# Performance work log

Hardware: AMD Instinct MI355X
Metric: run time of the kernel (lower is better)

The kernel has to match this reference:

```python
import jax, jax.numpy as jnp
import numpy as np

N, E, F_IN, C, H, L, G, OUT = 10000, 120000, 64, 128, 4, 5, 500, 1801
HL = (L * C) // 2  # JK bidirectional LSTM hidden per direction = 320


def setup_inputs():
    key = jax.random.key(0)
    ks = jax.random.split(key, 20)
    s = 0.05
    p = {}
    p["x"] = jax.random.normal(ks[0], (N, F_IN), jnp.float32)
    p["edge_index"] = jax.random.randint(ks[1], (2, E), 0, N)
    p["batch"] = jnp.sort(jax.random.randint(ks[2], (N,), 0, G))
    p["emb_W"] = jax.random.normal(ks[3], (F_IN, C)) * s
    p["emb_b"] = jnp.zeros((C,))
    p["Wl"] = jax.random.normal(ks[4], (L, C, H * C)) * s
    p["bl"] = jnp.zeros((L, H * C))
    p["Wr"] = jax.random.normal(ks[5], (L, C, H * C)) * s
    p["br"] = jnp.zeros((L, H * C))
    p["att_a"] = jax.random.normal(ks[6], (L, H, C)) * s
    p["conv_b"] = jnp.zeros((L, C))
    p["ln_w"] = jnp.ones((L, C))
    p["ln_b"] = jnp.zeros((L, C))
    p["Wih_f"] = jax.random.normal(ks[7], (4 * HL, C)) * s
    p["Whh_f"] = jax.random.normal(ks[8], (4 * HL, HL)) * s
    p["bih_f"] = jnp.zeros((4 * HL,))
    p["bhh_f"] = jnp.zeros((4 * HL,))
    p["Wih_b"] = jax.random.normal(ks[9], (4 * HL, C)) * s
    p["Whh_b"] = jax.random.normal(ks[10], (4 * HL, HL)) * s
    p["bih_b"] = jnp.zeros((4 * HL,))
    p["bhh_b"] = jnp.zeros((4 * HL,))
    p["jk_w"] = jax.random.normal(ks[11], (2 * HL,)) * s
    p["jk_b"] = jnp.zeros(())
    p["m1_w"] = jax.random.normal(ks[12], (C, C)) * s
    p["m1_b"] = jnp.zeros((C,))
    p["m2_w"] = jax.random.normal(ks[13], (C, OUT)) * s
    p["m2_b"] = jnp.zeros((OUT,))
    p["res_w"] = jax.random.normal(ks[14], (C, OUT)) * s
    p["res_b"] = jnp.zeros((OUT,))
    return p


def _layernorm(x, w, b):
    mu = x.mean(-1, keepdims=True)
    var = ((x - mu) ** 2).mean(-1, keepdims=True)
    return (x - mu) * jax.lax.rsqrt(var + 1e-5) * w + b


def _gatv2(x, src, dst, Wl, bl, Wr, br, a, bias):
    # GATv2Conv, concat=False: mean over heads; eval mode (no dropout)
    xl = (x @ Wl + bl).reshape(N, H, C)   # source projection
    xr = (x @ Wr + br).reshape(N, H, C)   # target projection
    xj = xl[src]                          # [E,H,C] messages from source
    e = jax.nn.leaky_relu(xj + xr[dst], 0.2)
    score = jnp.einsum('ehc,hc->eh', e, a)              # [E,H]
    m = jax.ops.segment_max(score, dst, num_segments=N)  # per-target max
    m = jnp.where(jnp.isfinite(m), m, 0.0)
    ex = jnp.exp(score - m[dst])
    denom = jax.ops.segment_sum(ex, dst, num_segments=N)
    alpha = ex / (denom[dst] + 1e-16)                   # PyG segment softmax
    out = jax.ops.segment_sum(xj * alpha[:, :, None], dst, num_segments=N)
    return out.mean(axis=1) + bias


def _lstm(seq, Wih, Whh, bih, bhh):
    # seq: [L, N, C]; torch gate order i,f,g,o
    def step(carry, xt):
        h, c = carry
        g = xt @ Wih.T + bih + h @ Whh.T + bhh
        i, f, gg, o = jnp.split(g, 4, axis=-1)
        c = jax.nn.sigmoid(f) * c + jax.nn.sigmoid(i) * jnp.tanh(gg)
        h = jax.nn.sigmoid(o) * jnp.tanh(c)
        return (h, c), h
    h0 = jnp.zeros((seq.shape[1], HL), seq.dtype)
    _, hs = jax.lax.scan(step, (h0, h0), seq)
    return hs


def reference(x, edge_index, batch, emb_W, emb_b, Wl, bl, Wr, br, att_a, conv_b, ln_w, ln_b, Wih_f, Whh_f, bih_f, bhh_f, Wih_b, Whh_b, bih_b, bhh_b, jk_w, jk_b, m1_w, m1_b, m2_w, m2_b, res_w, res_b):
    src, dst = edge_index[0], edge_index[1]
    h = x @ emb_W + emb_b
    xs = []
    for l in range(L):
        h = _gatv2(h, src, dst, Wl[l], bl[l], Wr[l], br[l], att_a[l], conv_b[l])
        h = _layernorm(h, ln_w[l], ln_b[l])
        xs.append(h)
    seq = jnp.stack(xs, axis=0)                           # [L,N,C]
    hf = _lstm(seq, Wih_f, Whh_f, bih_f, bhh_f)
    hb = _lstm(seq[::-1], Wih_b, Whh_b, bih_b, bhh_b)[::-1]
    feat = jnp.concatenate([hf, hb], axis=-1)             # [L,N,2*HL]
    scores = feat @ jk_w + jk_b                           # [L,N]
    alpha = jax.nn.softmax(scores, axis=0)
    node = (seq * alpha[:, :, None]).sum(axis=0)          # [N,C]
    cnt = jax.ops.segment_sum(jnp.ones((N,), node.dtype), batch, num_segments=G)
    pooled = jax.ops.segment_sum(node, batch, num_segments=G) / jnp.maximum(cnt, 1.0)[:, None]
    hdn = jax.nn.relu(pooled @ m1_w + m1_b)               # MLPBlock (eval: no dropout)
    return hdn @ m2_w + m2_b + pooled @ res_w + res_b
```

## Files before the change

kernel.cpp:

```cpp
#include <hip/hip_runtime.h>
#include <hip/hip_bf16.h>
#include <math.h>

constexpr int cN   = 10000;
constexpr int cE   = 120000;
constexpr int cFin = 64;
constexpr int cC   = 128;
constexpr int cH   = 4;
constexpr int cL   = 5;
constexpr int cG   = 500;
constexpr int cOUT = 1801;
constexpr int cHL  = 320;
constexpr int c4HL = 4 * cHL;

typedef short bf16x8 __attribute__((ext_vector_type(8)));
typedef float f32x4 __attribute__((ext_vector_type(4)));

__device__ inline unsigned short f2b(float x) {
    union { __hip_bfloat16 h; unsigned short u; } cv;
    cv.h = __float2bfloat16(x);
    return cv.u;
}
__device__ inline float b2f(unsigned short u) {
    union { unsigned int i; float f; } cv;
    cv.i = ((unsigned int)u) << 16;
    return cv.f;
}
__device__ inline float fsig(float x)  { return 1.f / (1.f + __expf(-x)); }
__device__ inline float ftanh(float x) { return 1.f - 2.f / (__expf(2.f * x) + 1.f); }

#define GLD16(g, l) __builtin_amdgcn_global_load_lds( \
    (const __attribute__((address_space(1))) unsigned int*)(g), \
    (__attribute__((address_space(3))) unsigned int*)(l), 16, 0, 0)

__global__ void fill_f32_kernel(float* __restrict__ p, long n, float v) {
    long i = (long)blockIdx.x * blockDim.x + threadIdx.x;
    if (i < n) p[i] = v;
}
__global__ void fill_i32_kernel(int* __restrict__ p, long n, int v) {
    long i = (long)blockIdx.x * blockDim.x + threadIdx.x;
    if (i < n) p[i] = v;
}
__global__ void copy_i32_kernel(const int* __restrict__ a, int* __restrict__ b, long n) {
    long i = (long)blockIdx.x * blockDim.x + threadIdx.x;
    if (i < n) b[i] = a[i];
}
__global__ void conv_bf16_kernel(const float* __restrict__ a, unsigned short* __restrict__ b, long n) {
    long i = (long)blockIdx.x * blockDim.x + threadIdx.x;
    if (i < n) b[i] = f2b(a[i]);
}
__global__ void wproj_prep_kernel(const float* __restrict__ Wl, const float* __restrict__ Wr,
                                  unsigned short* __restrict__ WT) {
    long i = (long)blockIdx.x * blockDim.x + threadIdx.x;
    if (i >= (long)cL * 1024 * 128) return;
    int k = i & 127;
    int n = (int)((i >> 7) & 1023);
    int l = (int)(i >> 17);
    const float* W = (n < 512) ? Wl : Wr;
    int nn = n & 511;
    WT[i] = f2b(W[(size_t)l * 65536 + (size_t)k * 512 + nn]);
}
__global__ void bias_prep_kernel(const float* __restrict__ bl, const float* __restrict__ br,
                                 float* __restrict__ bb) {
    int i = blockIdx.x * blockDim.x + threadIdx.x;
    if (i >= cL * 1024) return;
    int n = i & 1023, l = i >> 10;
    bb[i] = (n < 512) ? bl[l * 512 + n] : br[l * 512 + (n - 512)];
}
__global__ void embw_prep_kernel(const float* __restrict__ W, unsigned short* __restrict__ WT) {
    int i = blockIdx.x * blockDim.x + threadIdx.x;
    if (i >= cC * cFin) return;
    int k = i & 63, n = i >> 6;
    WT[i] = f2b(W[(size_t)k * cC + n]);
}
__global__ void lstm_prep_kernel(const float* __restrict__ Wih, const float* __restrict__ Whh,
                                 const float* __restrict__ bih, const float* __restrict__ bhh,
                                 unsigned short* __restrict__ WihP, unsigned short* __restrict__ WhhP,
                                 float* __restrict__ biasP) {
    long i = (long)blockIdx.x * blockDim.x + threadIdx.x;
    if (i >= (long)c4HL * 449) return;
    int p = (int)(i / 449), c = (int)(i % 449);
    int u = (p >> 6) * 16 + (p & 15);
    int g = (p >> 4) & 3;
    int r = g * cHL + u;
    if (c < cC)       WihP[(size_t)p * cC + c] = f2b(Wih[(size_t)r * cC + c]);
    else if (c < 448) WhhP[(size_t)p * cHL + (c - cC)] = f2b(Whh[(size_t)r * cHL + (c - cC)]);
    else              biasP[p] = bih[r] + bhh[r];
}

__global__ void hist_kernel(const int* __restrict__ dst, int* __restrict__ count) {
    int i = blockIdx.x * blockDim.x + threadIdx.x;
    if (i < cE) atomicAdd(&count[dst[i]], 1);
}
__global__ void scan_kernel(const int* __restrict__ count, int* __restrict__ offs) {
    __shared__ int part[256];
    const int tid = threadIdx.x;
    const int CH = (cN + 255) / 256;
    int base = tid * CH;
    int s = 0;
    for (int i = 0; i < CH; i++) {
        int idx = base + i;
        if (idx < cN) s += count[idx];
    }
    part[tid] = s;
    __syncthreads();
    for (int d = 1; d < 256; d <<= 1) {
        int v = 0;
        if (tid >= d) v = part[tid - d];
        __syncthreads();
        if (tid >= d) part[tid] += v;
        __syncthreads();
    }
    int prefix = (tid == 0) ? 0 : part[tid - 1];
    for (int i = 0; i < CH; i++) {
        int idx = base + i;
        if (idx < cN) { offs[idx] = prefix; prefix += count[idx]; }
    }
    if (tid == 255) offs[cN] = prefix;
}
__global__ void scatter_kernel(const int* __restrict__ src, const int* __restrict__ dst,
                               int* __restrict__ cursor, int* __restrict__ src_csr) {
    int i = blockIdx.x * blockDim.x + threadIdx.x;
    if (i < cE) {
        int pos = atomicAdd(&cursor[dst[i]], 1);
        src_csr[pos] = src[i];
    }
}

template<int HASBIAS, int OUTB, int SWZ>
__global__ __launch_bounds__(256)
void gemm_mfma_kernel(const unsigned short* __restrict__ A1, const unsigned short* __restrict__ B1, int k1,
                      const unsigned short* __restrict__ A2, const unsigned short* __restrict__ B2, int k2,
                      const float* __restrict__ bias, void* __restrict__ Cout, int M, int N, int nbn) {
    int bm, bn;
    if (SWZ) {
        int bid = blockIdx.x;
        int xcd = bid & 7, j = bid >> 3;
        int g   = (j / nbn) * 8 + xcd;
        bm = g << 7;
        bn = (j % nbn) << 7;
        if (bm >= M) return;
    } else {
        bm = blockIdx.y << 7;
        bn = blockIdx.x << 7;
    }
    __shared__ unsigned short lds[2][2][128 * 32];
    const int tid  = threadIdx.x;
    const int lane = tid & 63;
    const int wave = tid >> 6;
    const int wr = (wave >> 1) << 6;
    const int wc = (wave & 1) << 6;
    const int ns1 = k1 >> 5, ns2 = k2 >> 5, ns = ns1 + ns2;

    const int lrow = lane >> 2;
    const int lke  = (lane & 3) << 3;

    auto stage = [&](int s, int buf) {
        const unsigned short *Ab, *Bb;
        int stride, koff;
        if (s < ns1) { Ab = A1; Bb = B1; stride = k1; koff = s << 5; }
        else         { Ab = A2; Bb = B2; stride = k2; koff = (s - ns1) << 5; }
#pragma unroll
        for (int r = 0; r < 2; r++) {
            int ch  = wave * 2 + r;
            int row = ch * 16 + lrow;
            int ga  = bm + row; if (ga >= M) ga = M - 1;
            GLD16(Ab + (size_t)ga * stride + koff + lke, &lds[buf][0][ch * 512]);
            GLD16(Bb + (size_t)(bn + row) * stride + koff + lke, &lds[buf][1][ch * 512]);
        }
    };

    f32x4 acc[4][4];
#pragma unroll
    for (int i = 0; i < 4; i++)
#pragma unroll
        for (int j = 0; j < 4; j++) acc[i][j] = (f32x4){0.f, 0.f, 0.f, 0.f};

    stage(0, 0);
    const int ko  = (lane >> 4) << 3;
    const int rla = lane & 15;
    for (int s = 0; s < ns; s++) {
        int buf = s & 1;
        __syncthreads();
        if (s + 1 < ns) stage(s + 1, buf ^ 1);
        bf16x8 af[4], bff[4];
#pragma unroll
        for (int f = 0; f < 4; f++) {
            af[f]  = *(const bf16x8*)&lds[buf][0][(wr + f * 16 + rla) * 32 + ko];
            bff[f] = *(const bf16x8*)&lds[buf][1][(wc + f * 16 + rla) * 32 + ko];
        }
#pragma unroll
        for (int i = 0; i < 4; i++)
#pragma unroll
            for (int j = 0; j < 4; j++)
                acc[i][j] = __builtin_amdgcn_mfma_f32_16x16x32_bf16(af[i], bff[j], acc[i][j], 0, 0, 0);
    }

#pragma unroll
    for (int i = 0; i < 4; i++) {
#pragma unroll
        for (int v = 0; v < 4; v++) {
            int m = bm + wr + i * 16 + ((lane >> 4) << 2) + v;
            if (m < M) {
#pragma unroll
                for (int j = 0; j < 4; j++) {
                    int n = bn + wc + j * 16 + rla;
                    float val = acc[i][j][v];
                    if (HASBIAS) val += bias[n];
                    if (OUTB) ((unsigned short*)Cout)[(size_t)m * N + n] = f2b(val);
                    else      ((float*)Cout)[(size_t)m * N + n] = val;
                }
            }
        }
    }
}

template<int FIRST>
__global__ __launch_bounds__(512)
void gemm_lstm_dual_kernel(const unsigned short* __restrict__ A1f, const unsigned short* __restrict__ A1b,
                           const unsigned short* __restrict__ Bihf, const unsigned short* __restrict__ Bihb,
                           const unsigned short* __restrict__ A2f, const unsigned short* __restrict__ A2b,
                           const unsigned short* __restrict__ Bhhf, const unsigned short* __restrict__ Bhhb,
                           const float* __restrict__ biasPf, const float* __restrict__ biasPb,
                           float* __restrict__ cff, float* __restrict__ cbb,
                           unsigned short* __restrict__ hOutf, unsigned short* __restrict__ hOutb,
                           const float* __restrict__ jkw,
                           float* __restrict__ scoref, float* __restrict__ scoreb) {
    constexpr int M = cN, k1 = cC, k2 = FIRST ? 0 : cHL;
    const int bid = blockIdx.x;
    const int xcd = bid & 7, jj = bid >> 3;
    const int g     = (jj / 10) * 8 + xcd;
    const int inner = jj % 10;
    const int bm = g << 7;
    if (bm >= M) return;
    const int bn = (inner % 5) << 8;
    const int z  = inner / 5;

    const unsigned short* A1 = z ? A1b : A1f;
    const unsigned short* B1 = z ? Bihb : Bihf;
    const unsigned short* A2 = z ? A2b : A2f;
    const unsigned short* B2 = z ? Bhhb : Bhhf;
    const float* biasP = z ? biasPb : biasPf;
    float* cbuf = z ? cbb : cff;
    unsigned short* hOut = z ? hOutb : hOutf;
    const float* jkwz = jkw + (z ? cHL : 0);
    float* score_t = z ? scoreb : scoref;

    __shared__ unsigned short ldsA[2][128 * 32];
    __shared__ unsigned short ldsB[2][256 * 32];
    const int tid  = threadIdx.x;
    const int lane = tid & 63;
    const int wave = tid >> 6;
    const int wr = (wave >> 2) << 6;
    const int wc = (wave & 3) << 6;
    const int ns1 = k1 >> 5, ns2 = k2 >> 5, ns = ns1 + ns2;

    const int lrow = lane >> 2;
    const int lke  = (lane & 3) << 3;

    auto stage = [&](int s, int buf) {
        const unsigned short *Ab, *Bb;
        int stride, koff;
        if (s < ns1) { Ab = A1; Bb = B1; stride = k1; koff = s << 5; }
        else         { Ab = A2; Bb = B2; stride = k2; koff = (s - ns1) << 5; }
        {
            int row = wave * 16 + lrow;
            int ga  = bm + row; if (ga >= M) ga = M - 1;
            GLD16(Ab + (size_t)ga * stride + koff + lke, &ldsA[buf][wave * 512]);
        }
#pragma unroll
        for (int r = 0; r < 2; r++) {
            int ch  = wave * 2 + r;
            int row = ch * 16 + lrow;
            GLD16(Bb + (size_t)(bn + row) * stride + koff + lke, &ldsB[buf][ch * 512]);
        }
    };

    f32x4 acc[4][4];
#pragma unroll
    for (int i = 0; i < 4; i++)
#pragma unroll
        for (int j = 0; j < 4; j++) acc[i][j] = (f32x4){0.f, 0.f, 0.f, 0.f};

    stage(0, 0);
    const int ko  = (lane >> 4) << 3;
    const int rla = lane & 15;
    for (int s = 0; s < ns; s++) {
        int buf = s & 1;
        __syncthreads();
        if (s + 1 < ns) stage(s + 1, buf ^ 1);
        bf16x8 af[4], bff[4];
#pragma unroll
        for (int f = 0; f < 4; f++) {
            af[f]  = *(const bf16x8*)&ldsA[buf][(wr + f * 16 + rla) * 32 + ko];
            bff[f] = *(const bf16x8*)&ldsB[buf][(wc + f * 16 + rla) * 32 + ko];
        }
#pragma unroll
        for (int i = 0; i < 4; i++)
#pragma unroll
            for (int j = 0; j < 4; j++)
                acc[i][j] = __builtin_amdgcn_mfma_f32_16x16x32_bf16(af[i], bff[j], acc[i][j], 0, 0, 0);
    }

    float bias4[4];
#pragma unroll
    for (int j = 0; j < 4; j++) bias4[j] = biasP[bn + wc + j * 16 + rla];
    const int u = ((bn + wc) >> 6) * 16 + rla;
    const float jw = jkwz[u];

#pragma unroll
    for (int i = 0; i < 4; i++) {
#pragma unroll
        for (int v = 0; v < 4; v++) {
            int m = bm + wr + i * 16 + ((lane >> 4) << 2) + v;
            bool ok = (m < M);
            float gi = acc[i][0][v] + bias4[0];
            float gf = acc[i][1][v] + bias4[1];
            float gg = acc[i][2][v] + bias4[2];
            float go = acc[i][3][v] + bias4[3];
            float si = fsig(gi);
            float sf = fsig(gf);
            float so = fsig(go);
            float tg = ftanh(gg);
            size_t idx = (size_t)m * cHL + u;
            float cold = (FIRST || !ok) ? 0.f : cbuf[idx];
            float cc = sf * cold + si * tg;
            float hh = so * ftanh(cc);
            if (ok) { cbuf[idx] = cc; hOut[idx] = f2b(hh); }
            float part = ok ? hh * jw : 0.f;
#pragma unroll
            for (int o = 1; o < 16; o <<= 1) part += __shfl_xor(part, o);
            if (rla == 0 && ok) atomicAdd(&score_t[m], part);
        }
    }
}

__global__ __launch_bounds__(256)
void gat_fused_kernel(const unsigned short* __restrict__ xlr, const int* __restrict__ src_csr,
                      const int* __restrict__ offs, const float* __restrict__ att,
                      const float* __restrict__ conv_b, const float* __restrict__ lnw,
                      const float* __restrict__ lnb, float* __restrict__ seq_l,
                      unsigned short* __restrict__ seqb_l) {
    const int wv   = (blockIdx.x * blockDim.x + threadIdx.x) >> 6;
    const int lane = threadIdx.x & 63;
    if (wv >= cN) return;
    const int h   = lane >> 4;
    const int cb  = (lane & 15) << 3;

    bf16x8 xrv = *(const bf16x8*)&xlr[(size_t)wv * 1024 + 512 + lane * 8];
    float xr[8], av[8];
#pragma unroll
    for (int k = 0; k < 8; k++) {
        xr[k] = b2f((unsigned short)xrv[k]);
        av[k] = att[h * 128 + cb + k];
    }

    float m = -INFINITY, l = 0.f;
    float acc[8];
#pragma unroll
    for (int k = 0; k < 8; k++) acc[k] = 0.f;

    const int beg = offs[wv], end = offs[wv + 1];
    int j = beg;
    for (; j + 1 < end; j += 2) {
        int s0 = src_csr[j], s1 = src_csr[j + 1];
        bf16x8 xv0 = *(const bf16x8*)&xlr[(size_t)s0 * 1024 + lane * 8];
        bf16x8 xv1 = *(const bf16x8*)&xlr[(size_t)s1 * 1024 + lane * 8];
        float x0[8], x1[8], sc0 = 0.f, sc1 = 0.f;
#pragma unroll
        for (int k = 0; k < 8; k++) {
            x0[k] = b2f((unsigned short)xv0[k]);
            float v0 = x0[k] + xr[k];
            v0 = v0 > 0.f ? v0 : 0.2f * v0;
            sc0 = fmaf(v0, av[k], sc0);
            x1[k] = b2f((unsigned short)xv1[k]);
            float v1 = x1[k] + xr[k];
            v1 = v1 > 0.f ? v1 : 0.2f * v1;
            sc1 = fmaf(v1, av[k], sc1);
        }
#pragma unroll
        for (int o = 1; o < 16; o <<= 1) {
            sc0 += __shfl_xor(sc0, o);
            sc1 += __shfl_xor(sc1, o);
        }
        float mn = fmaxf(m, fmaxf(sc0, sc1));
        float r  = __expf(m - mn);
        float p0 = __expf(sc0 - mn);
        float p1 = __expf(sc1 - mn);
        l = l * r + p0 + p1;
#pragma unroll
        for (int k = 0; k < 8; k++)
            acc[k] = fmaf(acc[k], r, fmaf(p0, x0[k], p1 * x1[k]));
        m = mn;
    }
    if (j < end) {
        int s0 = src_csr[j];
        bf16x8 xv = *(const bf16x8*)&xlr[(size_t)s0 * 1024 + lane * 8];
        float x[8], sc = 0.f;
#pragma unroll
        for (int k = 0; k < 8; k++) {
            x[k] = b2f((unsigned short)xv[k]);
            float v = x[k] + xr[k];
            v = v > 0.f ? v : 0.2f * v;
            sc = fmaf(v, av[k], sc);
        }
#pragma unroll
        for (int o = 1; o < 16; o <<= 1) sc += __shfl_xor(sc, o);
        float mn = fmaxf(m, sc);
        float r  = __expf(m - mn);
        float p  = __expf(sc - mn);
        l = l * r + p;
#pragma unroll
        for (int k = 0; k < 8; k++) acc[k] = fmaf(acc[k], r, p * x[k]);
        m = mn;
    }
    float inv = 1.f / (l + 1e-16f);

#pragma unroll
    for (int k = 0; k < 8; k++) {
        float v = acc[k] * inv;
        v += __shfl_xor(v, 16);
        v += __shfl_xor(v, 32);
        acc[k] = 0.25f * v + conv_b[cb + k];
    }
    float ssum = 0.f;
#pragma unroll
    for (int k = 0; k < 8; k++) ssum += acc[k];
#pragma unroll
    for (int o = 1; o < 16; o <<= 1) ssum += __shfl_xor(ssum, o);
    float mu = ssum * (1.f / 128.f);
    float vs = 0.f;
#pragma unroll
    for (int k = 0; k < 8; k++) { float d = acc[k] - mu; vs = fmaf(d, d, vs); }
#pragma unroll
    for (int o = 1; o < 16; o <<= 1) vs += __shfl_xor(vs, o);
    float rstd = 1.f / sqrtf(vs * (1.f / 128.f) + 1e-5f);

    float outv[8];
#pragma unroll
    for (int k = 0; k < 8; k++)
        outv[k] = (acc[k] - mu) * rstd * lnw[cb + k] + lnb[cb + k];

    if (h == 0) {
        size_t b = (size_t)wv * 128 + cb;
        float4 o0 = make_float4(outv[0], outv[1], outv[2], outv[3]);
        float4 o1 = make_float4(outv[4], outv[5], outv[6], outv[7]);
        *(float4*)&seq_l[b]     = o0;
        *(float4*)&seq_l[b + 4] = o1;
        bf16x8 ob;
#pragma unroll
        for (int k = 0; k < 8; k++) ob[k] = (short)f2b(outv[k]);
        *(bf16x8*)&seqb_l[b] = ob;
    }
}

__global__ void jk_pool_kernel(const float* __restrict__ seq, const float* __restrict__ score,
                               const int* __restrict__ batch, float* __restrict__ pooled) {
    int wid = (blockIdx.x * blockDim.x + threadIdx.x) >> 6;
    int lane = threadIdx.x & 63;
    if (wid >= cN) return;
    float s[cL], mx = -INFINITY;
#pragma unroll
    for (int l = 0; l < cL; l++) { s[l] = score[(size_t)l * cN + wid]; mx = fmaxf(mx, s[l]); }
    float se = 0.f;
#pragma unroll
    for (int l = 0; l < cL; l++) { s[l] = __expf(s[l] - mx); se += s[l]; }
    float inv = 1.f / se;
    int g = batch[wid];
    float acc0 = 0.f, acc1 = 0.f;
#pragma unroll
    for (int l = 0; l < cL; l++) {
        const float* sp = seq + ((size_t)l * cN + wid) * 128;
        float w = s[l] * inv;
        acc0 += w * sp[lane];
        acc1 += w * sp[lane + 64];
    }
    atomicAdd(&pooled[(size_t)g * 128 + lane], acc0);
    atomicAdd(&pooled[(size_t)g * 128 + lane + 64], acc1);
}

__global__ void count_kernel(const int* __restrict__ batch, float* __restrict__ cnt) {
    int i = blockIdx.x * blockDim.x + threadIdx.x;
    if (i < cN) atomicAdd(&cnt[batch[i]], 1.f);
}

__global__ void div_pool_kernel(float* __restrict__ pooled, const float* __restrict__ cnt) {
    int i = blockIdx.x * blockDim.x + threadIdx.x;
    if (i < cG * 128) pooled[i] /= fmaxf(cnt[i >> 7], 1.f);
}

__global__ __launch_bounds__(256)
void head_fused_kernel(const float* __restrict__ pooled,
                       const float* __restrict__ m1_w, const float* __restrict__ m1_b,
                       const float* __restrict__ m2_w, const float* __restrict__ m2_b,
                       const float* __restrict__ res_w, const float* __restrict__ res_b,
                       float* __restrict__ out) {
    __shared__ float pl[4][128];
    __shared__ float hd[4][128];
    const int tid = threadIdx.x;
    const int r0 = blockIdx.y << 2;
    const int c0 = blockIdx.x << 8;
#pragma unroll
    for (int e = tid; e < 512; e += 256) {
        int r = e >> 7, k = e & 127;
        pl[r][k] = pooled[(size_t)(r0 + r) * 128 + k];
    }
    __syncthreads();
#pragma unroll
    for (int e = tid; e < 512; e += 256) {
        int r = e >> 7, n = e & 127;
        float acc = m1_b[n];
#pragma unroll 8
        for (int k = 0; k < 128; k++) acc = fmaf(pl[r][k], m1_w[k * 128 + n], acc);
        hd[r][n] = fmaxf(acc, 0.f);
    }
    __syncthreads();
    int col = c0 + tid;
    if (col >= cOUT) return;
    float b = m2_b[col] + res_b[col];
    float acc[4] = {b, b, b, b};
    for (int k = 0; k < 128; k++) {
        float w2 = m2_w[(size_t)k * cOUT + col];
        float wr = res_w[(size_t)k * cOUT + col];
#pragma unroll
        for (int r = 0; r < 4; r++)
            acc[r] = fmaf(hd[r][k], w2, fmaf(pl[r][k], wr, acc[r]));
    }
#pragma unroll
    for (int r = 0; r < 4; r++)
        out[(size_t)(r0 + r) * cOUT + col] = acc[r];
}

static inline int ceil_div(long a, long b) { return (int)((a + b - 1) / b); }

template<int OUTB>
static void launch_mfma(const unsigned short* A1, const unsigned short* B1, int k1,
                        const unsigned short* A2, const unsigned short* B2, int k2,
                        const float* bias, void* C, int M, int N, hipStream_t s) {
    dim3 g((N + 127) >> 7, (M + 127) >> 7);
    if (bias) gemm_mfma_kernel<1, OUTB, 0><<<g, 256, 0, s>>>(A1, B1, k1, A2, B2, k2, bias, C, M, N, 0);
    else      gemm_mfma_kernel<0, OUTB, 0><<<g, 256, 0, s>>>(A1, B1, k1, A2, B2, k2, bias, C, M, N, 0);
}
template<int OUTB>
static void launch_mfma_swz(const unsigned short* A1, const unsigned short* B1, int k1,
                            const float* bias, void* C, int M, int N, hipStream_t s) {
    int nbn = N >> 7;
    int groups = ((((M + 127) >> 7) + 7) / 8) * 8;
    dim3 g(groups * nbn);
    gemm_mfma_kernel<1, OUTB, 1><<<g, 256, 0, s>>>(A1, B1, k1, nullptr, nullptr, 0, bias, C, M, N, nbn);
}

static void fillF(float* p, long n, float v, hipStream_t s) {
    fill_f32_kernel<<<ceil_div(n, 256), 256, 0, s>>>(p, n, v);
}
static void fillI(int* p, long n, int v, hipStream_t s) {
    fill_i32_kernel<<<ceil_div(n, 256), 256, 0, s>>>(p, n, v);
}
static void convB(const float* a, unsigned short* b, long n, hipStream_t s) {
    conv_bf16_kernel<<<ceil_div(n, 256), 256, 0, s>>>(a, b, n);
}

extern "C" void kernel_launch(void* const* d_in, const int* in_sizes, int n_in,
                              void* d_out, int out_size, void* d_ws, size_t ws_size,
                              hipStream_t stream) {
    const float* x      = (const float*)d_in[0];
    const int*   ei     = (const int*)d_in[1];
    const int*   batch  = (const int*)d_in[2];
    const float* emb_W  = (const float*)d_in[3];
    const float* emb_b  = (const float*)d_in[4];
    const float* Wl     = (const float*)d_in[5];
    const float* bl     = (const float*)d_in[6];
    const float* Wr     = (const float*)d_in[7];
    const float* br     = (const float*)d_in[8];
    const float* att_a  = (const float*)d_in[9];
    const float* conv_b = (const float*)d_in[10];
    const float* ln_w   = (const float*)d_in[11];
    const float* ln_b   = (const float*)d_in[12];
    const float* Wih_f  = (const float*)d_in[13];
    const float* Whh_f  = (const float*)d_in[14];
    const float* bih_f  = (const float*)d_in[15];
    const float* bhh_f  = (const float*)d_in[16];
    const float* Wih_b  = (const float*)d_in[17];
    const float* Whh_b  = (const float*)d_in[18];
    const float* bih_b  = (const float*)d_in[19];
    const float* bhh_b  = (const float*)d_in[20];
    const float* jk_w   = (const float*)d_in[21];
    const float* m1_w   = (const float*)d_in[23];
    const float* m1_b   = (const float*)d_in[24];
    const float* m2_w   = (const float*)d_in[25];
    const float* m2_b   = (const float*)d_in[26];
    const float* res_w  = (const float*)d_in[27];
    const float* res_b  = (const float*)d_in[28];
    float* out = (float*)d_out;

    const int* src = ei;
    const int* dst = ei + cE;

    char* ws = (char*)d_ws;
    size_t off = 0;
    auto alloc = [&](size_t bytes) -> char* {
        size_t o = (off + 255) & ~(size_t)255;
        off = o + bytes;
        return ws + o;
    };
    unsigned short* x16     = (unsigned short*)alloc((size_t)cN * cFin * 2);
    unsigned short* embWT   = (unsigned short*)alloc((size_t)cC * cFin * 2);
    unsigned short* emb_b16 = (unsigned short*)alloc((size_t)cN * cC * 2);
    float*          seq     = (float*)alloc((size_t)cL * cN * cC * 4);
    unsigned short* seqb16  = (unsigned short*)alloc((size_t)cL * cN * cC * 2);
    unsigned short* WT      = (unsigned short*)alloc((size_t)cL * 1024 * 128 * 2);
    float*          bb      = (float*)alloc((size_t)cL * 1024 * 4);
    unsigned short* WihPf   = (unsigned short*)alloc((size_t)c4HL * cC * 2);
    unsigned short* WhhPf   = (unsigned short*)alloc((size_t)c4HL * cHL * 2);
    unsigned short* WihPb   = (unsigned short*)alloc((size_t)c4HL * cC * 2);
    unsigned short* WhhPb   = (unsigned short*)alloc((size_t)c4HL * cHL * 2);
    float*          biasPf  = (float*)alloc((size_t)c4HL * 4);
    float*          biasPb  = (float*)alloc((size_t)c4HL * 4);
    unsigned short* hf0     = (unsigned short*)alloc((size_t)cN * cHL * 2);
    unsigned short* hf1     = (unsigned short*)alloc((size_t)cN * cHL * 2);
    unsigned short* hbk0    = (unsigned short*)alloc((size_t)cN * cHL * 2);
    unsigned short* hbk1    = (unsigned short*)alloc((size_t)cN * cHL * 2);
    float*          cf      = (float*)alloc((size_t)cN * cHL * 4);
    float*          cbk     = (float*)alloc((size_t)cN * cHL * 4);
    float*          jks     = (float*)alloc((size_t)cL * cN * 4);
    float*          pooled  = (float*)alloc((size_t)cG * cC * 4);
    float*          cnt     = (float*)alloc((size_t)cG * 4);
    int*            offs    = (int*)alloc((size_t)(cN + 1) * 4);
    int*            cursor  = (int*)alloc((size_t)cN * 4);
    int*            src_csr = (int*)alloc((size_t)cE * 4);
    unsigned short* xlr     = (unsigned short*)alloc((size_t)cN * 1024 * 2);

    hipStream_t s = stream;

    fillI(cursor, cN, 0, s);
    hist_kernel<<<ceil_div(cE, 256), 256, 0, s>>>(dst, cursor);
    scan_kernel<<<1, 256, 0, s>>>(cursor, offs);
    copy_i32_kernel<<<ceil_div(cN, 256), 256, 0, s>>>(offs, cursor, cN);
    scatter_kernel<<<ceil_div(cE, 256), 256, 0, s>>>(src, dst, cursor, src_csr);

    wproj_prep_kernel<<<ceil_div((long)cL * 1024 * 128, 256), 256, 0, s>>>(Wl, Wr, WT);
    bias_prep_kernel<<<ceil_div((long)cL * 1024, 256), 256, 0, s>>>(bl, br, bb);
    embw_prep_kernel<<<ceil_div((long)cC * cFin, 256), 256, 0, s>>>(emb_W, embWT);
    convB(x, x16, (long)cN * cFin, s);
    lstm_prep_kernel<<<ceil_div((long)c4HL * 449, 256), 256, 0, s>>>(
        Wih_f, Whh_f, bih_f, bhh_f, WihPf, WhhPf, biasPf);
    lstm_prep_kernel<<<ceil_div((long)c4HL * 449, 256), 256, 0, s>>>(
        Wih_b, Whh_b, bih_b, bhh_b, WihPb, WhhPb, biasPb);

    launch_mfma<1>(x16, embWT, cFin, nullptr, nullptr, 0, emb_b, emb_b16, cN, cC, s);

    for (int l = 0; l < cL; l++) {
        const unsigned short* hin = (l == 0) ? emb_b16 : seqb16 + (size_t)(l - 1) * cN * cC;
        launch_mfma_swz<1>(hin, WT + (size_t)l * 1024 * 128, cC,
                           bb + (size_t)l * 1024, xlr, cN, 1024, s);
        gat_fused_kernel<<<ceil_div((long)cN * 64, 256), 256, 0, s>>>(
            xlr, src_csr, offs, att_a + (size_t)l * cH * cC,
            conv_b + (size_t)l * cC, ln_w + (size_t)l * cC, ln_b + (size_t)l * cC,
            seq + (size_t)l * cN * cC, seqb16 + (size_t)l * cN * cC);
    }

    fillF(jks, (long)cL * cN, 0.f, s);
    unsigned short* hfb[2]  = {hf0, hf1};
    unsigned short* hbb[2]  = {hbk0, hbk1};
    dim3 lg(80 * 10);
    for (int k = 0; k < cL; k++) {
        int cur = k & 1, prev = cur ^ 1;
        int t = cL - 1 - k;
        const unsigned short* A1f = seqb16 + (size_t)k * cN * cC;
        const unsigned short* A1b = seqb16 + (size_t)t * cN * cC;
        if (k == 0)
            gemm_lstm_dual_kernel<1><<<lg, 512, 0, s>>>(
                A1f, A1b, WihPf, WihPb, nullptr, nullptr, nullptr, nullptr,
                biasPf, biasPb, cf, cbk, hfb[cur], hbb[cur], jk_w,
                jks + (size_t)k * cN, jks + (size_t)t * cN);
        else
            gemm_lstm_dual_kernel<0><<<lg, 512, 0, s>>>(
                A1f, A1b, WihPf, WihPb, hfb[prev], hbb[prev], WhhPf, WhhPb,
                biasPf, biasPb, cf, cbk, hfb[cur], hbb[cur], jk_w,
                jks + (size_t)k * cN, jks + (size_t)t * cN);
    }

    fillF(pooled, (long)cG * cC, 0.f, s);
    fillF(cnt, cG, 0.f, s);
    jk_pool_kernel<<<ceil_div((long)cN * 64, 256), 256, 0, s>>>(seq, jks, batch, pooled);
    count_kernel<<<ceil_div(cN, 256), 256, 0, s>>>(batch, cnt);
    div_pool_kernel<<<ceil_div((long)cG * 128, 256), 256, 0, s>>>(pooled, cnt);
    head_fused_kernel<<<dim3(ceil_div(cOUT, 256), cG / 4), 256, 0, s>>>(
        pooled, m1_w, m1_b, m2_w, m2_b, res_w, res_b, out);
}
```

Baseline: 698.9 us.

## Precompute LSTM input projections in one batched GEMM, unroll GAT edges by four

Hoists the LSTM input-to-hidden projection for all timesteps and both directions into a single large bf16 GEMM over the stacked layer outputs. The per-step LSTM kernels then only run the recurrent GEMM and read the precomputed gate inputs from memory in the epilogue, which shortens the serial chain. The GAT aggregation loop now handles four edges per iteration instead of two, and three zero-fill launches are merged into one init kernel. In exchange it uses a large extra bf16 buffer and re-reads it from global memory, gated on workspace size.

```diff
diff --git a/kernel.cpp b/kernel.cpp
--- a/kernel.cpp
+++ b/kernel.cpp
@@ -12,6 +12,7 @@
 constexpr int cOUT = 1801;
 constexpr int cHL  = 320;
 constexpr int c4HL = 4 * cHL;
+constexpr int cP   = 2 * c4HL;
 
 typedef short bf16x8 __attribute__((ext_vector_type(8)));
 typedef float f32x4 __attribute__((ext_vector_type(4)));
@@ -33,10 +34,6 @@
     (const __attribute__((address_space(1))) unsigned int*)(g), \
     (__attribute__((address_space(3))) unsigned int*)(l), 16, 0, 0)
 
-__global__ void fill_f32_kernel(float* __restrict__ p, long n, float v) {
-    long i = (long)blockIdx.x * blockDim.x + threadIdx.x;
-    if (i < n) p[i] = v;
-}
 __global__ void fill_i32_kernel(int* __restrict__ p, long n, int v) {
     long i = (long)blockIdx.x * blockDim.x + threadIdx.x;
     if (i < n) p[i] = v;
@@ -48,6 +45,13 @@
 __global__ void conv_bf16_kernel(const float* __restrict__ a, unsigned short* __restrict__ b, long n) {
     long i = (long)blockIdx.x * blockDim.x + threadIdx.x;
     if (i < n) b[i] = f2b(a[i]);
+}
+__global__ void init_tail_kernel(float* __restrict__ jks, float* __restrict__ pooled,
+                                 float* __restrict__ cnt) {
+    long i = (long)blockIdx.x * blockDim.x + threadIdx.x;
+    if (i < (long)cL * cN) jks[i] = 0.f;
+    else if (i < (long)cL * cN + cG * cC) pooled[i - (long)cL * cN] = 0.f;
+    else if (i < (long)cL * cN + cG * cC + cG) cnt[i - (long)cL * cN - cG * cC] = 0.f;
 }
 __global__ void wproj_prep_kernel(const float* __restrict__ Wl, const float* __restrict__ Wr,
                                   unsigned short* __restrict__ WT) {
@@ -215,7 +219,7 @@
     }
 }
 
-template<int FIRST>
+template<int FIRST, int USEP>
 __global__ __launch_bounds__(512)
 void gemm_lstm_dual_kernel(const unsigned short* __restrict__ A1f, const unsigned short* __restrict__ A1b,
                            const unsigned short* __restrict__ Bihf, const unsigned short* __restrict__ Bihb,
@@ -225,8 +229,11 @@
                            float* __restrict__ cff, float* __restrict__ cbb,
                            unsigned short* __restrict__ hOutf, unsigned short* __restrict__ hOutb,
                            const float* __restrict__ jkw,
-                           float* __restrict__ scoref, float* __restrict__ scoreb) {
-    constexpr int M = cN, k1 = cC, k2 = FIRST ? 0 : cHL;
+                           float* __restrict__ scoref, float* __restrict__ scoreb,
+                           const unsigned short* __restrict__ PfP, const unsigned short* __restrict__ PbP) {
+    constexpr int M = cN;
+    constexpr int k1 = USEP ? 0 : cC;
+    constexpr int k2 = FIRST ? 0 : cHL;
     const int bid = blockIdx.x;
     const int xcd = bid & 7, jj = bid >> 3;
     const int g     = (jj / 10) * 8 + xcd;
@@ -245,6 +252,8 @@
     unsigned short* hOut = z ? hOutb : hOutf;
     const float* jkwz = jkw + (z ? cHL : 0);
     float* score_t = z ? scoreb : scoref;
+    const unsigned short* Pst = z ? PbP : PfP;
+    const int pcb = (z ? c4HL : 0) + bn;
 
     __shared__ unsigned short ldsA[2][128 * 32];
     __shared__ unsigned short ldsB[2][256 * 32];
@@ -282,7 +291,7 @@
 #pragma unroll
         for (int j = 0; j < 4; j++) acc[i][j] = (f32x4){0.f, 0.f, 0.f, 0.f};
 
-    stage(0, 0);
+    if (ns > 0) stage(0, 0);
     const int ko  = (lane >> 4) << 3;
     const int rla = lane & 15;
     for (int s = 0; s < ns; s++) {
@@ -314,10 +323,17 @@
         for (int v = 0; v < 4; v++) {
             int m = bm + wr + i * 16 + ((lane >> 4) << 2) + v;
             bool ok = (m < M);
-            float gi = acc[i][0][v] + bias4[0];
-            float gf = acc[i][1][v] + bias4[1];
-            float gg = acc[i][2][v] + bias4[2];
-            float go = acc[i][3][v] + bias4[3];
+            float p4[4] = {0.f, 0.f, 0.f, 0.f};
+            if (USEP) {
+                int mp = ok ? m : M - 1;
+#pragma unroll
+                for (int j = 0; j < 4; j++)
+                    p4[j] = b2f(Pst[(size_t)mp * cP + pcb + wc + j * 16 + rla]);
+            }
+            float gi = acc[i][0][v] + p4[0] + bias4[0];
+            float gf = acc[i][1][v] + p4[1] + bias4[1];
+            float gg = acc[i][2][v] + p4[2] + bias4[2];
+            float go = acc[i][3][v] + p4[3] + bias4[3];
             float si = fsig(gi);
             float sf = fsig(gf);
             float so = fsig(go);
@@ -362,38 +378,50 @@
 
     const int beg = offs[wv], end = offs[wv + 1];
     int j = beg;
-    for (; j + 1 < end; j += 2) {
-        int s0 = src_csr[j], s1 = src_csr[j + 1];
+    for (; j + 3 < end; j += 4) {
+        int s0 = src_csr[j], s1 = src_csr[j + 1], s2 = src_csr[j + 2], s3 = src_csr[j + 3];
         bf16x8 xv0 = *(const bf16x8*)&xlr[(size_t)s0 * 1024 + lane * 8];
         bf16x8 xv1 = *(const bf16x8*)&xlr[(size_t)s1 * 1024 + lane * 8];
-        float x0[8], x1[8], sc0 = 0.f, sc1 = 0.f;
+        bf16x8 xv2 = *(const bf16x8*)&xlr[(size_t)s2 * 1024 + lane * 8];
+        bf16x8 xv3 = *(const bf16x8*)&xlr[(size_t)s3 * 1024 + lane * 8];
+        float x0[8], x1[8], x2[8], x3[8];
+        float sc0 = 0.f, sc1 = 0.f, sc2 = 0.f, sc3 = 0.f;
 #pragma unroll
         for (int k = 0; k < 8; k++) {
             x0[k] = b2f((unsigned short)xv0[k]);
-            float v0 = x0[k] + xr[k];
-            v0 = v0 > 0.f ? v0 : 0.2f * v0;
+            x1[k] = b2f((unsigned short)xv1[k]);
+            x2[k] = b2f((unsigned short)xv2[k]);
+            x3[k] = b2f((unsigned short)xv3[k]);
+            float v0 = x0[k] + xr[k]; v0 = v0 > 0.f ? v0 : 0.2f * v0;
+            float v1 = x1[k] + xr[k]; v1 = v1 > 0.f ? v1 : 0.2f * v1;
+            float v2 = x2[k] + xr[k]; v2 = v2 > 0.f ? v2 : 0.2f * v2;
+            float v3 = x3[k] + xr[k]; v3 = v3 > 0.f ? v3 : 0.2f * v3;
             sc0 = fmaf(v0, av[k], sc0);
-            x1[k] = b2f((unsigned short)xv1[k]);
-            float v1 = x1[k] + xr[k];
-            v1 = v1 > 0.f ? v1 : 0.2f * v1;
             sc1 = fmaf(v1, av[k], sc1);
+            sc2 = fmaf(v2, av[k], sc2);
+            sc3 = fmaf(v3, av[k], sc3);
         }
 #pragma unroll
         for (int o = 1; o < 16; o <<= 1) {
             sc0 += __shfl_xor(sc0, o);
             sc1 += __shfl_xor(sc1, o);
-        }
-        float mn = fmaxf(m, fmaxf(sc0, sc1));
+            sc2 += __shfl_xor(sc2, o);
+            sc3 += __shfl_xor(sc3, o);
+        }
+        float mn = fmaxf(fmaxf(fmaxf(sc0, sc1), fmaxf(sc2, sc3)), m);
         float r  = __expf(m - mn);
         float p0 = __expf(sc0 - mn);
         float p1 = __expf(sc1 - mn);
-        l = l * r + p0 + p1;
+        float p2 = __expf(sc2 - mn);
+        float p3 = __expf(sc3 - mn);
+        l = l * r + p0 + p1 + p2 + p3;
 #pragma unroll
         for (int k = 0; k < 8; k++)
-            acc[k] = fmaf(acc[k], r, fmaf(p0, x0[k], p1 * x1[k]));
+            acc[k] = fmaf(acc[k], r,
+                          fmaf(p0, x0[k], fmaf(p1, x1[k], fmaf(p2, x2[k], p3 * x3[k]))));
         m = mn;
     }
-    if (j < end) {
+    for (; j < end; j++) {
         int s0 = src_csr[j];
         bf16x8 xv = *(const bf16x8*)&xlr[(size_t)s0 * 1024 + lane * 8];
         float x[8], sc = 0.f;
@@ -541,18 +569,15 @@
     if (bias) gemm_mfma_kernel<1, OUTB, 0><<<g, 256, 0, s>>>(A1, B1, k1, A2, B2, k2, bias, C, M, N, 0);
     else      gemm_mfma_kernel<0, OUTB, 0><<<g, 256, 0, s>>>(A1, B1, k1, A2, B2, k2, bias, C, M, N, 0);
 }
-template<int OUTB>
+template<int HASBIAS, int OUTB>
 static void launch_mfma_swz(const unsigned short* A1, const unsigned short* B1, int k1,
                             const float* bias, void* C, int M, int N, hipStream_t s) {
     int nbn = N >> 7;
     int groups = ((((M + 127) >> 7) + 7) / 8) * 8;
     dim3 g(groups * nbn);
-    gemm_mfma_kernel<1, OUTB, 1><<<g, 256, 0, s>>>(A1, B1, k1, nullptr, nullptr, 0, bias, C, M, N, nbn);
-}
-
-static void fillF(float* p, long n, float v, hipStream_t s) {
-    fill_f32_kernel<<<ceil_div(n, 256), 256, 0, s>>>(p, n, v);
-}
+    gemm_mfma_kernel<HASBIAS, OUTB, 1><<<g, 256, 0, s>>>(A1, B1, k1, nullptr, nullptr, 0, bias, C, M, N, nbn);
+}
+
 static void fillI(int* p, long n, int v, hipStream_t s) {
     fill_i32_kernel<<<ceil_div(n, 256), 256, 0, s>>>(p, n, v);
 }
@@ -610,9 +635,8 @@
     unsigned short* seqb16  = (unsigned short*)alloc((size_t)cL * cN * cC * 2);
     unsigned short* WT      = (unsigned short*)alloc((size_t)cL * 1024 * 128 * 2);
     float*          bb      = (float*)alloc((size_t)cL * 1024 * 4);
-    unsigned short* WihPf   = (unsigned short*)alloc((size_t)c4HL * cC * 2);
+    unsigned short* WihPfb  = (unsigned short*)alloc((size_t)cP * cC * 2);
     unsigned short* WhhPf   = (unsigned short*)alloc((size_t)c4HL * cHL * 2);
-    unsigned short* WihPb   = (unsigned short*)alloc((size_t)c4HL * cC * 2);
     unsigned short* WhhPb   = (unsigned short*)alloc((size_t)c4HL * cHL * 2);
     float*          biasPf  = (float*)alloc((size_t)c4HL * 4);
     float*          biasPb  = (float*)alloc((size_t)c4HL * 4);
@@ -629,6 +653,11 @@
     int*            cursor  = (int*)alloc((size_t)cN * 4);
     int*            src_csr = (int*)alloc((size_t)cE * 4);
     unsigned short* xlr     = (unsigned short*)alloc((size_t)cN * 1024 * 2);
+    unsigned short* Pall    = (unsigned short*)alloc((size_t)cL * cN * cP * 2);
+    const bool useP = (off <= ws_size);
+
+    unsigned short* WihPf = WihPfb;
+    unsigned short* WihPb = WihPfb + (size_t)c4HL * cC;
 
     hipStream_t s = stream;
 
@@ -646,20 +675,23 @@
         Wih_f, Whh_f, bih_f, bhh_f, WihPf, WhhPf, biasPf);
     lstm_prep_kernel<<<ceil_div((long)c4HL * 449, 256), 256, 0, s>>>(
         Wih_b, Whh_b, bih_b, bhh_b, WihPb, WhhPb, biasPb);
+    init_tail_kernel<<<ceil_div((long)cL * cN + cG * cC + cG, 256), 256, 0, s>>>(jks, pooled, cnt);
 
     launch_mfma<1>(x16, embWT, cFin, nullptr, nullptr, 0, emb_b, emb_b16, cN, cC, s);
 
     for (int l = 0; l < cL; l++) {
         const unsigned short* hin = (l == 0) ? emb_b16 : seqb16 + (size_t)(l - 1) * cN * cC;
-        launch_mfma_swz<1>(hin, WT + (size_t)l * 1024 * 128, cC,
-                           bb + (size_t)l * 1024, xlr, cN, 1024, s);
+        launch_mfma_swz<1, 1>(hin, WT + (size_t)l * 1024 * 128, cC,
+                              bb + (size_t)l * 1024, xlr, cN, 1024, s);
         gat_fused_kernel<<<ceil_div((long)cN * 64, 256), 256, 0, s>>>(
             xlr, src_csr, offs, att_a + (size_t)l * cH * cC,
             conv_b + (size_t)l * cC, ln_w + (size_t)l * cC, ln_b + (size_t)l * cC,
             seq + (size_t)l * cN * cC, seqb16 + (size_t)l * cN * cC);
     }
 
-    fillF(jks, (long)cL * cN, 0.f, s);
+    if (useP) {
+        launch_mfma_swz<0, 1>(seqb16, WihPfb, cC, nullptr, Pall, cL * cN, cP, s);
+    }
     unsigned short* hfb[2]  = {hf0, hf1};
     unsigned short* hbb[2]  = {hbk0, hbk1};
     dim3 lg(80 * 10);
@@ -668,20 +700,33 @@
         int t = cL - 1 - k;
         const unsigned short* A1f = seqb16 + (size_t)k * cN * cC;
         const unsigned short* A1b = seqb16 + (size_t)t * cN * cC;
-        if (k == 0)
-            gemm_lstm_dual_kernel<1><<<lg, 512, 0, s>>>(
-                A1f, A1b, WihPf, WihPb, nullptr, nullptr, nullptr, nullptr,
-                biasPf, biasPb, cf, cbk, hfb[cur], hbb[cur], jk_w,
-                jks + (size_t)k * cN, jks + (size_t)t * cN);
-        else
-            gemm_lstm_dual_kernel<0><<<lg, 512, 0, s>>>(
-                A1f, A1b, WihPf, WihPb, hfb[prev], hbb[prev], WhhPf, WhhPb,
-                biasPf, biasPb, cf, cbk, hfb[cur], hbb[cur], jk_w,
-                jks + (size_t)k * cN, jks + (size_t)t * cN);
-    }
-
-    fillF(pooled, (long)cG * cC, 0.f, s);
-    fillF(cnt, cG, 0.f, s);
+        const unsigned short* PfP = Pall + (size_t)k * cN * cP;
+        const unsigned short* PbP = Pall + (size_t)t * cN * cP;
+        if (useP) {
+            if (k == 0)
+                gemm_lstm_dual_kernel<1, 1><<<lg, 512, 0, s>>>(
+                    nullptr, nullptr, nullptr, nullptr, nullptr, nullptr, nullptr, nullptr,
+                    biasPf, biasPb, cf, cbk, hfb[cur], hbb[cur], jk_w,
+                    jks + (size_t)k * cN, jks + (size_t)t * cN, PfP, PbP);
+            else
+                gemm_lstm_dual_kernel<0, 1><<<lg, 512, 0, s>>>(
+                    nullptr, nullptr, nullptr, nullptr, hfb[prev], hbb[prev], WhhPf, WhhPb,
+                    biasPf, biasPb, cf, cbk, hfb[cur], hbb[cur], jk_w,
+                    jks + (size_t)k * cN, jks + (size_t)t * cN, PfP, PbP);
+        } else {
+            if (k == 0)
+                gemm_lstm_dual_kernel<1, 0><<<lg, 512, 0, s>>>(
+                    A1f, A1b, WihPf, WihPb, nullptr, nullptr, nullptr, nullptr,
+                    biasPf, biasPb, cf, cbk, hfb[cur], hbb[cur], jk_w,
+                    jks + (size_t)k * cN, jks + (size_t)t * cN, nullptr, nullptr);
+            else
+                gemm_lstm_dual_kernel<0, 0><<<lg, 512, 0, s>>>(
+                    A1f, A1b, WihPf, WihPb, hfb[prev], hbb[prev], WhhPf, WhhPb,
+                    biasPf, biasPb, cf, cbk, hfb[cur], hbb[cur], jk_w,
+                    jks + (size_t)k * cN, jks + (size_t)t * cN, nullptr, nullptr);
+        }
+    }
+
     jk_pool_kernel<<<ceil_div((long)cN * 64, 256), 256, 0, s>>>(seq, jks, batch, pooled);
     count_kernel<<<ceil_div(cN, 256), 256, 0, s>>>(batch, cnt);
     div_pool_kernel<<<ceil_div((long)cG * 128, 256), 256, 0, s>>>(pooled, cnt);
```

After: 683.5 us. 2.2% less time.
